# Optimization experiments

Measured on AMD Instinct MI355X. Metric: run time of the kernel, lower is better.

The kernel has to match this reference:

```python
import jax, jax.numpy as jnp
import numpy as np
import math

B, S, D = 8, 2048, 512
H, DH = 8, 64  # heads, head dim

def setup_inputs() -> dict:
    key = jax.random.key(0)
    ks = jax.random.split(key, 13)
    w = 0.02
    return {
        "x_Q": jax.random.normal(ks[0], (B, S, D), jnp.float32),
        "x_K": jax.random.normal(ks[1], (B, S, D), jnp.float32),
        "x_V": jax.random.normal(ks[2], (B, S, D), jnp.float32),
        "Wq": jax.random.normal(ks[3], (H * DH, D), jnp.float32) * w,
        "bq": jnp.zeros((H * DH,), jnp.float32),
        "Wk": jax.random.normal(ks[4], (H * DH, D), jnp.float32) * w,
        "bk": jnp.zeros((H * DH,), jnp.float32),
        "Wv": jax.random.normal(ks[5], (H * DH, D), jnp.float32) * w,
        "bv": jnp.zeros((H * DH,), jnp.float32),
        "Wo": jax.random.normal(ks[6], (D, H * DH), jnp.float32) * w,
        "bo": jnp.zeros((D,), jnp.float32),
        "src_batch_lens": jax.random.randint(ks[7], (B,), 1, S + 1, jnp.int32),
    }

def reference(x_Q, x_K, x_V, Wq, bq, Wk, bk, Wv, bv, Wo, bo, src_batch_lens):
    b, s, _ = x_Q.shape
    # projections (torch Linear: x @ W.T + b), split into heads
    Q = (x_Q @ Wq.T + bq).reshape(b, s, H, DH)
    K = (x_K @ Wk.T + bk).reshape(b, s, H, DH)
    V = (x_V @ Wv.T + bv).reshape(b, s, H, DH)
    scale = 1.0 / math.sqrt(DH)
    # [b, h, q, k] scores
    scores = jnp.einsum('bqhd,bkhd->bhqk', Q * scale, K)
    # padding mask on key positions >= src_batch_lens[i], filled with -1e9
    key_mask = jnp.arange(s)[None, :] >= src_batch_lens[:, None]  # [b, k]
    scores = jnp.where(key_mask[:, None, None, :], -1.0e9, scores)
    attn = jax.nn.softmax(scores, axis=-1)  # dropout p=0.0 -> identity
    ctx = jnp.einsum('bhqk,bkhd->bqhd', attn, V).reshape(b, s, H * DH)
    return ctx @ Wo.T + bo
```

## Files before the change

kernel.cpp:

```cpp
#include <hip/hip_runtime.h>
#include <math.h>

#define NB 8
#define NS 2048
#define ND 512
#define NHH 8
#define NDH 64

typedef __attribute__((ext_vector_type(4))) float f32x4;
typedef __attribute__((ext_vector_type(8))) short bf16x8;
typedef unsigned short ush;

__device__ inline ush f2bf_rne(float f) {
    unsigned u = __float_as_uint(f);
    unsigned r = u + 0x7FFFu + ((u >> 16) & 1u);
    return (ush)(r >> 16);
}
__device__ inline float bf2f(ush h) { return __uint_as_float(((unsigned)h) << 16); }

__device__ inline unsigned cvt_pk_bf16(float lo, float hi) {
    unsigned r;
    asm("v_cvt_pk_bf16_f32 %0, %1, %2" : "=v"(r) : "v"(lo), "v"(hi));
    return r;
}

#if defined(__has_builtin)
#if __has_builtin(__builtin_amdgcn_exp2f)
#define EXP2F(x) __builtin_amdgcn_exp2f(x)
#else
#define EXP2F(x) exp2f(x)
#endif
#else
#define EXP2F(x) exp2f(x)
#endif

#define GLL16(gp, lp) __builtin_amdgcn_global_load_lds( \
    (const __attribute__((address_space(1))) unsigned int*)(gp), \
    (__attribute__((address_space(3))) unsigned int*)(lp), 16, 0, 0)

__global__ __launch_bounds__(256) void conv_w_kernel(
    const float* __restrict__ Wq, const float* __restrict__ Wk,
    const float* __restrict__ Wv, const float* __restrict__ Wo,
    ush* __restrict__ wbf, ush* __restrict__ wo_hi, ush* __restrict__ wo_lo)
{
    const int y = blockIdx.y;
    const int i = (blockIdx.x * 256 + threadIdx.x) * 4;
    if (y < 3) {
        const float* src = (y == 0) ? Wq : (y == 1) ? Wk : Wv;
        const float4 v = *(const float4*)&src[i];
        ushort4 o;
        o.x = f2bf_rne(v.x); o.y = f2bf_rne(v.y);
        o.z = f2bf_rne(v.z); o.w = f2bf_rne(v.w);
        *(ushort4*)&wbf[y * 262144 + i] = o;
    } else {
        const float4 v = *(const float4*)&Wo[i];
        ushort4 hi, lo;
        hi.x = f2bf_rne(v.x); lo.x = f2bf_rne(v.x - bf2f(hi.x));
        hi.y = f2bf_rne(v.y); lo.y = f2bf_rne(v.y - bf2f(hi.y));
        hi.z = f2bf_rne(v.z); lo.z = f2bf_rne(v.z - bf2f(hi.z));
        hi.w = f2bf_rne(v.w); lo.w = f2bf_rne(v.w - bf2f(hi.w));
        *(ushort4*)&wo_hi[i] = hi;
        *(ushort4*)&wo_lo[i] = lo;
    }
}

__global__ __launch_bounds__(256) void qkv_gemm_kernel(
    const float* __restrict__ xq, const float* __restrict__ xk, const float* __restrict__ xv,
    const ush* __restrict__ wbf,
    const float* __restrict__ bq, const float* __restrict__ bk, const float* __restrict__ bv,
    ush* __restrict__ Qb, ush* __restrict__ Kb, ush* __restrict__ VT)
{
    __shared__ ush As[4096];
    __shared__ ush Bs[4096];

    const int z = blockIdx.z;
    const float* X    = (z == 0) ? xq : (z == 1) ? xk : xv;
    const ush*   W    = wbf + z * 262144;
    const float* bias = (z == 0) ? bq : (z == 1) ? bk : bv;

    const int t = threadIdx.x;
    const int w = t >> 6, l = t & 63;
    const int l15 = l & 15, g = l >> 4;
    const int m0 = blockIdx.x * 128, n0 = blockIdx.y * 128;
    const int wm = (w & 1) << 6, wn = (w >> 1) << 6;

    const int srow = l >> 2;
    const int sg   = (l & 3) ^ ((srow + (srow >> 2)) & 3);
    const int fsw  = (g ^ ((l15 + (l15 >> 2)) & 3)) << 3;
    const int c0   = w * 2;

    f32x4 acc[4][4];
    #pragma unroll
    for (int i = 0; i < 4; ++i)
        #pragma unroll
        for (int j = 0; j < 4; ++j) acc[i][j] = (f32x4)(0.0f);

    for (int kt = 0; kt < 512; kt += 32) {
        const size_t ar0 = (size_t)(m0 + c0 * 16 + srow) * 512 + kt + sg * 8;
        const size_t ar1 = (size_t)(m0 + (c0 + 1) * 16 + srow) * 512 + kt + sg * 8;
        const float4 a0 = *(const float4*)&X[ar0];
        const float4 a1 = *(const float4*)&X[ar0 + 4];
        const float4 a2 = *(const float4*)&X[ar1];
        const float4 a3 = *(const float4*)&X[ar1 + 4];

        __syncthreads();

        GLL16(&W[(size_t)(n0 + c0 * 16 + srow) * 512 + kt + sg * 8], &Bs[c0 * 512 + l * 8]);
        GLL16(&W[(size_t)(n0 + (c0 + 1) * 16 + srow) * 512 + kt + sg * 8], &Bs[(c0 + 1) * 512 + l * 8]);

        uint4 u0, u1;
        u0.x = (unsigned)f2bf_rne(a0.x) | ((unsigned)f2bf_rne(a0.y) << 16);
        u0.y = (unsigned)f2bf_rne(a0.z) | ((unsigned)f2bf_rne(a0.w) << 16);
        u0.z = (unsigned)f2bf_rne(a1.x) | ((unsigned)f2bf_rne(a1.y) << 16);
        u0.w = (unsigned)f2bf_rne(a1.z) | ((unsigned)f2bf_rne(a1.w) << 16);
        u1.x = (unsigned)f2bf_rne(a2.x) | ((unsigned)f2bf_rne(a2.y) << 16);
        u1.y = (unsigned)f2bf_rne(a2.z) | ((unsigned)f2bf_rne(a2.w) << 16);
        u1.z = (unsigned)f2bf_rne(a3.x) | ((unsigned)f2bf_rne(a3.y) << 16);
        u1.w = (unsigned)f2bf_rne(a3.z) | ((unsigned)f2bf_rne(a3.w) << 16);
        *(uint4*)&As[c0 * 512 + l * 8] = u0;
        *(uint4*)&As[(c0 + 1) * 512 + l * 8] = u1;

        __syncthreads();

        bf16x8 af[4], bfr[4];
        #pragma unroll
        for (int mi = 0; mi < 4; ++mi)
            af[mi] = *(const bf16x8*)&As[(((w & 1) << 2) + mi) * 512 + l15 * 32 + fsw];
        #pragma unroll
        for (int ni = 0; ni < 4; ++ni)
            bfr[ni] = *(const bf16x8*)&Bs[(((w >> 1) << 2) + ni) * 512 + l15 * 32 + fsw];
        #pragma unroll
        for (int mi = 0; mi < 4; ++mi)
            #pragma unroll
            for (int ni = 0; ni < 4; ++ni)
                acc[mi][ni] = __builtin_amdgcn_mfma_f32_16x16x32_bf16(af[mi], bfr[ni], acc[mi][ni], 0, 0, 0);
    }

    const float qscale = (z == 0) ? 0.18033688011112042f : 1.0f;
    float bnv[4];
    #pragma unroll
    for (int ni = 0; ni < 4; ++ni) bnv[ni] = bias[n0 + wn + ni * 16 + l15];

    if (z < 2) {
        ush* O = (z == 0) ? Qb : Kb;
        #pragma unroll
        for (int mi = 0; mi < 4; ++mi) {
            #pragma unroll
            for (int ni = 0; ni < 4; ++ni) {
                const int n = n0 + wn + ni * 16 + l15;
                const int hh = n >> 6, dh = n & 63;
                #pragma unroll
                for (int r = 0; r < 4; ++r) {
                    const int m = m0 + wm + mi * 16 + (g << 2) + r;
                    const int bi = m >> 11, s = m & (NS - 1);
                    O[((size_t)(bi * 8 + hh) * 2048 + s) * 64 + dh] =
                        f2bf_rne((acc[mi][ni][r] + bnv[ni]) * qscale);
                }
            }
        }
    } else {
        #pragma unroll
        for (int mi = 0; mi < 4; ++mi) {
            #pragma unroll
            for (int ni = 0; ni < 4; ++ni) {
                const int n = n0 + wn + ni * 16 + l15;
                const int hh = n >> 6, dh = n & 63;
                const int mb = m0 + wm + mi * 16 + (g << 2);
                const int bi = mb >> 11, s = mb & (NS - 1);
                ushort4 pk;
                pk.x = f2bf_rne(acc[mi][ni][0] + bnv[ni]);
                pk.y = f2bf_rne(acc[mi][ni][1] + bnv[ni]);
                pk.z = f2bf_rne(acc[mi][ni][2] + bnv[ni]);
                pk.w = f2bf_rne(acc[mi][ni][3] + bnv[ni]);
                *(ushort4*)&VT[((size_t)(bi * 8 + hh) * 64 + dh) * 2048 + s] = pk;
            }
        }
    }
}

__global__ __launch_bounds__(256) void attn_kernel(
    ush* __restrict__ Qb, const ush* __restrict__ Kb,
    const ush* __restrict__ VT, const int* __restrict__ lens,
    ush* __restrict__ ctx_lo)
{
    __shared__ ush Ps[64 * 72];
    __shared__ ush Vt[2 * 4624];

    const int tid = threadIdx.x;
    const int w = tid >> 6, l = tid & 63;
    const int l15 = l & 15, g = l >> 4;

    const int id = blockIdx.x;
    const int h = id & 7, qt = (id >> 3) & 31, b = id >> 8;
    const int L = lens[b];
    const int q0 = qt << 6;
    const size_t bh = ((size_t)b * 8 + h) * 2048;

    const ush* qptr = Qb + (bh + q0 + w * 16 + l15) * 64 + g * 8;
    const bf16x8 qf0 = *(const bf16x8*)(qptr);
    const bf16x8 qf1 = *(const bf16x8*)(qptr + 32);

    const ush* kbase = Kb + (bh + l15) * 64 + g * 8;

    const int dv = tid >> 2, seg = (tid & 3) << 4;
    const ush* vbase = VT + bh * 64 + (size_t)dv * 2048 + seg;
    const int vt_off = dv * 72 + ((dv >> 4) << 3) + seg;

    ush* psw = &Ps[(w * 16 + l15) * 72 + (g << 2)];
    const ush* pp = &Ps[(w * 16 + l15) * 72 + g * 8];

    bf16x8 ones;
    #pragma unroll
    for (int j = 0; j < 8; ++j) ones[j] = (short)0x3F80;

    f32x4 o[4];
    f32x4 ol = (f32x4)(0.0f);
    #pragma unroll
    for (int i = 0; i < 4; ++i) o[i] = (f32x4)(0.0f);

    f32x4 sp[4];
    const int T = (L + 63) >> 6;

    {
        const uint4 v0 = *(const uint4*)(vbase);
        const uint4 v1 = *(const uint4*)(vbase + 8);
        #pragma unroll
        for (int st = 0; st < 4; ++st) sp[st] = (f32x4)(0.0f);
        __builtin_amdgcn_s_setprio(1);
        #pragma unroll
        for (int st = 0; st < 4; ++st) {
            const bf16x8 kf0 = *(const bf16x8*)(kbase + st * 1024);
            const bf16x8 kf1 = *(const bf16x8*)(kbase + st * 1024 + 32);
            sp[st] = __builtin_amdgcn_mfma_f32_16x16x32_bf16(kf0, qf0, sp[st], 0, 0, 0);
            sp[st] = __builtin_amdgcn_mfma_f32_16x16x32_bf16(kf1, qf1, sp[st], 0, 0, 0);
        }
        __builtin_amdgcn_s_setprio(0);
        ush* dst = &Vt[vt_off];
        *(uint4*)dst = v0;
        *(uint4*)(dst + 8) = v1;
        __syncthreads();
    }

    auto finish = [&](const ush* vb, bool masked, int kb0) {
        uint2 pk[4];
        #pragma unroll
        for (int st = 0; st < 4; ++st) {
            float p[4];
            #pragma unroll
            for (int r = 0; r < 4; ++r) {
                float e = EXP2F(sp[st][r]);
                if (masked) {
                    const int key = kb0 + st * 16 + (g << 2) + r;
                    e = (key < L) ? e : 0.0f;
                }
                p[r] = e;
            }
            pk[st].x = cvt_pk_bf16(p[0], p[1]);
            pk[st].y = cvt_pk_bf16(p[2], p[3]);
        }
        #pragma unroll
        for (int st = 0; st < 4; ++st)
            *(uint2*)(psw + st * 16) = pk[st];
        const bf16x8 pf0 = *(const bf16x8*)(pp);
        const bf16x8 pf1 = *(const bf16x8*)(pp + 32);
        __builtin_amdgcn_s_setprio(1);
        ol = __builtin_amdgcn_mfma_f32_16x16x32_bf16(pf0, ones, ol, 0, 0, 0);
        ol = __builtin_amdgcn_mfma_f32_16x16x32_bf16(pf1, ones, ol, 0, 0, 0);
        #pragma unroll
        for (int st2 = 0; st2 < 4; ++st2) {
            const ush* vp = vb + (st2 * 16 + l15) * 72 + (st2 << 3) + g * 8;
            const bf16x8 vf0 = *(const bf16x8*)(vp);
            const bf16x8 vf1 = *(const bf16x8*)(vp + 32);
            o[st2] = __builtin_amdgcn_mfma_f32_16x16x32_bf16(pf0, vf0, o[st2], 0, 0, 0);
            o[st2] = __builtin_amdgcn_mfma_f32_16x16x32_bf16(pf1, vf1, o[st2], 0, 0, 0);
        }
        __builtin_amdgcn_s_setprio(0);
    };

    for (int t = 1; t < T; ++t) {
        const int k0 = t << 6;
        const uint4 nv0 = *(const uint4*)(vbase + k0);
        const uint4 nv1 = *(const uint4*)(vbase + k0 + 8);
        bf16x8 kf[8];
        const ush* kp = kbase + (size_t)k0 * 64;
        #pragma unroll
        for (int st = 0; st < 4; ++st) {
            kf[2 * st]     = *(const bf16x8*)(kp + st * 1024);
            kf[2 * st + 1] = *(const bf16x8*)(kp + st * 1024 + 32);
        }

        finish(&Vt[((t & 1) ^ 1) * 4624], false, 0);

        #pragma unroll
        for (int st = 0; st < 4; ++st) sp[st] = (f32x4)(0.0f);
        __builtin_amdgcn_s_setprio(1);
        #pragma unroll
        for (int st = 0; st < 4; ++st) {
            sp[st] = __builtin_amdgcn_mfma_f32_16x16x32_bf16(kf[2 * st], qf0, sp[st], 0, 0, 0);
            sp[st] = __builtin_amdgcn_mfma_f32_16x16x32_bf16(kf[2 * st + 1], qf1, sp[st], 0, 0, 0);
        }
        __builtin_amdgcn_s_setprio(0);

        ush* dst = &Vt[(t & 1) * 4624 + vt_off];
        *(uint4*)dst = nv0;
        *(uint4*)(dst + 8) = nv1;
        __syncthreads();
    }

    finish(&Vt[((T - 1) & 1) * 4624], true, (T - 1) << 6);

    #pragma unroll
    for (int r = 0; r < 4; ++r) {
        const float inv = 1.0f / ol[r];
        const size_t row = bh + q0 + w * 16 + (g << 2) + r;
        #pragma unroll
        for (int st2 = 0; st2 < 4; ++st2) {
            const float val = o[st2][r] * inv;
            const ush hi = f2bf_rne(val);
            const ush lo = f2bf_rne(val - bf2f(hi));
            Qb[row * 64 + st2 * 16 + l15] = hi;
            ctx_lo[row * 64 + st2 * 16 + l15] = lo;
        }
    }
}

__global__ __launch_bounds__(256) void out_gemm_kernel(
    const ush* __restrict__ ctx_hi, const ush* __restrict__ ctx_lo,
    const ush* __restrict__ wo_hi, const ush* __restrict__ wo_lo,
    const float* __restrict__ bo, float* __restrict__ out)
{
    __shared__ ush Ah[4096], Al[4096], Bh[4096], Bl[4096];

    const int t = threadIdx.x;
    const int w = t >> 6, l = t & 63;
    const int l15 = l & 15, g = l >> 4;
    const int m0 = blockIdx.x * 128, n0 = blockIdx.y * 128;
    const int wm = (w & 1) << 6, wn = (w >> 1) << 6;

    const int srow = l >> 2;
    const int sg   = (l & 3) ^ ((srow + (srow >> 2)) & 3);
    const int fsw  = (g ^ ((l15 + (l15 >> 2)) & 3)) << 3;
    const int c0   = w * 2;

    f32x4 acc[4][4];
    #pragma unroll
    for (int i = 0; i < 4; ++i)
        #pragma unroll
        for (int j = 0; j < 4; ++j) acc[i][j] = (f32x4)(0.0f);

    for (int kt = 0; kt < 512; kt += 32) {
        __syncthreads();
        #pragma unroll
        for (int cc = 0; cc < 2; ++cc) {
            const int c = c0 + cc;
            const int m = m0 + c * 16 + srow;
            const int k = kt + sg * 8;
            const size_t ga = ((size_t)((m >> 11) * 8 + (k >> 6)) * 2048 + (m & (NS - 1))) * 64 + (k & 63);
            GLL16(&ctx_hi[ga], &Ah[c * 512 + l * 8]);
            GLL16(&ctx_lo[ga], &Al[c * 512 + l * 8]);
            const size_t gb = (size_t)(n0 + c * 16 + srow) * 512 + kt + sg * 8;
            GLL16(&wo_hi[gb], &Bh[c * 512 + l * 8]);
            GLL16(&wo_lo[gb], &Bl[c * 512 + l * 8]);
        }
        __syncthreads();

        bf16x8 ah[4], al[4], bh4[4], bl4[4];
        #pragma unroll
        for (int mi = 0; mi < 4; ++mi) {
            const int off = (((w & 1) << 2) + mi) * 512 + l15 * 32 + fsw;
            ah[mi] = *(const bf16x8*)&Ah[off];
            al[mi] = *(const bf16x8*)&Al[off];
        }
        #pragma unroll
        for (int ni = 0; ni < 4; ++ni) {
            const int off = (((w >> 1) << 2) + ni) * 512 + l15 * 32 + fsw;
            bh4[ni] = *(const bf16x8*)&Bh[off];
            bl4[ni] = *(const bf16x8*)&Bl[off];
        }
        #pragma unroll
        for (int mi = 0; mi < 4; ++mi)
            #pragma unroll
            for (int ni = 0; ni < 4; ++ni) {
                acc[mi][ni] = __builtin_amdgcn_mfma_f32_16x16x32_bf16(ah[mi], bh4[ni], acc[mi][ni], 0, 0, 0);
                acc[mi][ni] = __builtin_amdgcn_mfma_f32_16x16x32_bf16(al[mi], bh4[ni], acc[mi][ni], 0, 0, 0);
                acc[mi][ni] = __builtin_amdgcn_mfma_f32_16x16x32_bf16(ah[mi], bl4[ni], acc[mi][ni], 0, 0, 0);
            }
    }

    float bov[4];
    #pragma unroll
    for (int ni = 0; ni < 4; ++ni) bov[ni] = bo[n0 + wn + ni * 16 + l15];

    #pragma unroll
    for (int mi = 0; mi < 4; ++mi)
        #pragma unroll
        for (int ni = 0; ni < 4; ++ni) {
            const int n = n0 + wn + ni * 16 + l15;
            #pragma unroll
            for (int r = 0; r < 4; ++r) {
                const int m = m0 + wm + mi * 16 + (g << 2) + r;
                out[(size_t)m * 512 + n] = acc[mi][ni][r] + bov[ni];
            }
        }
}

extern "C" void kernel_launch(void* const* d_in, const int* in_sizes, int n_in,
                              void* d_out, int out_size, void* d_ws, size_t ws_size,
                              hipStream_t stream)
{
    const float* xq   = (const float*)d_in[0];
    const float* xk   = (const float*)d_in[1];
    const float* xv   = (const float*)d_in[2];
    const float* Wq   = (const float*)d_in[3];
    const float* bq   = (const float*)d_in[4];
    const float* Wk   = (const float*)d_in[5];
    const float* bk   = (const float*)d_in[6];
    const float* Wv   = (const float*)d_in[7];
    const float* bv   = (const float*)d_in[8];
    const float* Wo   = (const float*)d_in[9];
    const float* bo   = (const float*)d_in[10];
    const int*   lens = (const int*)d_in[11];
    float* out = (float*)d_out;

    const size_t elems = (size_t)NB * NHH * NS * NDH;
    ush* Qb     = (ush*)d_ws;
    ush* Kb     = Qb + elems;
    ush* VT     = Kb + elems;
    ush* ctx_lo = VT + elems;
    ush* wbf    = ctx_lo + elems;
    ush* wo_hi  = wbf + 3 * 262144;
    ush* wo_lo  = wo_hi + 262144;

    const dim3 blk(256);
    conv_w_kernel<<<dim3(256, 4), blk, 0, stream>>>(Wq, Wk, Wv, Wo, wbf, wo_hi, wo_lo);
    qkv_gemm_kernel<<<dim3(128, 4, 3), blk, 0, stream>>>(
        xq, xk, xv, wbf, bq, bk, bv, Qb, Kb, VT);
    attn_kernel<<<dim3(NB * NHH * (NS / 64)), blk, 0, stream>>>(Qb, Kb, VT, lens, ctx_lo);
    out_gemm_kernel<<<dim3(128, 4), blk, 0, stream>>>(Qb, ctx_lo, wo_hi, wo_lo, bo, out);
}
```

Measured before the change: 354.8 us.

## Double-buffer GEMM LDS tiles and process 128 queries per attention block

Both projection GEMMs now use double-buffered shared memory, so the next K-tile's global loads (and, in the QKV GEMM, the bf16 conversion) overlap the MFMAs on the current tile, with one barrier per iteration. The attention kernel now has each block handle two 64-row query tiles that share each staged K/V tile, halving K/V reloads and the block count. The cost is doubled LDS per block and more accumulator registers in attention, which may lower occupancy. Fewer attention blocks also makes load imbalance across variable sequence lengths worse.

```diff
diff --git a/kernel.cpp b/kernel.cpp
--- a/kernel.cpp
+++ b/kernel.cpp
@@ -70,8 +70,8 @@
     const float* __restrict__ bq, const float* __restrict__ bk, const float* __restrict__ bv,
     ush* __restrict__ Qb, ush* __restrict__ Kb, ush* __restrict__ VT)
 {
-    __shared__ ush As[4096];
-    __shared__ ush Bs[4096];
+    __shared__ ush As[2][4096];
+    __shared__ ush Bs[2][4096];
 
     const int z = blockIdx.z;
     const float* X    = (z == 0) ? xq : (z == 1) ? xk : xv;
@@ -95,19 +95,15 @@
         #pragma unroll
         for (int j = 0; j < 4; ++j) acc[i][j] = (f32x4)(0.0f);
 
-    for (int kt = 0; kt < 512; kt += 32) {
-        const size_t ar0 = (size_t)(m0 + c0 * 16 + srow) * 512 + kt + sg * 8;
-        const size_t ar1 = (size_t)(m0 + (c0 + 1) * 16 + srow) * 512 + kt + sg * 8;
+    {
+        const size_t ar0 = (size_t)(m0 + c0 * 16 + srow) * 512 + sg * 8;
+        const size_t ar1 = (size_t)(m0 + (c0 + 1) * 16 + srow) * 512 + sg * 8;
         const float4 a0 = *(const float4*)&X[ar0];
         const float4 a1 = *(const float4*)&X[ar0 + 4];
         const float4 a2 = *(const float4*)&X[ar1];
         const float4 a3 = *(const float4*)&X[ar1 + 4];
-
-        __syncthreads();
-
-        GLL16(&W[(size_t)(n0 + c0 * 16 + srow) * 512 + kt + sg * 8], &Bs[c0 * 512 + l * 8]);
-        GLL16(&W[(size_t)(n0 + (c0 + 1) * 16 + srow) * 512 + kt + sg * 8], &Bs[(c0 + 1) * 512 + l * 8]);
-
+        GLL16(&W[(size_t)(n0 + c0 * 16 + srow) * 512 + sg * 8], &Bs[0][c0 * 512 + l * 8]);
+        GLL16(&W[(size_t)(n0 + (c0 + 1) * 16 + srow) * 512 + sg * 8], &Bs[0][(c0 + 1) * 512 + l * 8]);
         uint4 u0, u1;
         u0.x = (unsigned)f2bf_rne(a0.x) | ((unsigned)f2bf_rne(a0.y) << 16);
         u0.y = (unsigned)f2bf_rne(a0.z) | ((unsigned)f2bf_rne(a0.w) << 16);
@@ -117,23 +113,53 @@
         u1.y = (unsigned)f2bf_rne(a2.z) | ((unsigned)f2bf_rne(a2.w) << 16);
         u1.z = (unsigned)f2bf_rne(a3.x) | ((unsigned)f2bf_rne(a3.y) << 16);
         u1.w = (unsigned)f2bf_rne(a3.z) | ((unsigned)f2bf_rne(a3.w) << 16);
-        *(uint4*)&As[c0 * 512 + l * 8] = u0;
-        *(uint4*)&As[(c0 + 1) * 512 + l * 8] = u1;
-
+        *(uint4*)&As[0][c0 * 512 + l * 8] = u0;
+        *(uint4*)&As[0][(c0 + 1) * 512 + l * 8] = u1;
         __syncthreads();
+    }
+
+    for (int ki = 0; ki < 16; ++ki) {
+        const int buf = ki & 1;
+        const int ktn = (ki + 1) * 32;
+        float4 a0, a1, a2, a3;
+        if (ki < 15) {
+            const size_t ar0 = (size_t)(m0 + c0 * 16 + srow) * 512 + ktn + sg * 8;
+            const size_t ar1 = (size_t)(m0 + (c0 + 1) * 16 + srow) * 512 + ktn + sg * 8;
+            a0 = *(const float4*)&X[ar0];
+            a1 = *(const float4*)&X[ar0 + 4];
+            a2 = *(const float4*)&X[ar1];
+            a3 = *(const float4*)&X[ar1 + 4];
+            GLL16(&W[(size_t)(n0 + c0 * 16 + srow) * 512 + ktn + sg * 8], &Bs[buf ^ 1][c0 * 512 + l * 8]);
+            GLL16(&W[(size_t)(n0 + (c0 + 1) * 16 + srow) * 512 + ktn + sg * 8], &Bs[buf ^ 1][(c0 + 1) * 512 + l * 8]);
+        }
 
         bf16x8 af[4], bfr[4];
         #pragma unroll
         for (int mi = 0; mi < 4; ++mi)
-            af[mi] = *(const bf16x8*)&As[(((w & 1) << 2) + mi) * 512 + l15 * 32 + fsw];
+            af[mi] = *(const bf16x8*)&As[buf][(((w & 1) << 2) + mi) * 512 + l15 * 32 + fsw];
         #pragma unroll
         for (int ni = 0; ni < 4; ++ni)
-            bfr[ni] = *(const bf16x8*)&Bs[(((w >> 1) << 2) + ni) * 512 + l15 * 32 + fsw];
+            bfr[ni] = *(const bf16x8*)&Bs[buf][(((w >> 1) << 2) + ni) * 512 + l15 * 32 + fsw];
         #pragma unroll
         for (int mi = 0; mi < 4; ++mi)
             #pragma unroll
             for (int ni = 0; ni < 4; ++ni)
                 acc[mi][ni] = __builtin_amdgcn_mfma_f32_16x16x32_bf16(af[mi], bfr[ni], acc[mi][ni], 0, 0, 0);
+
+        if (ki < 15) {
+            uint4 u0, u1;
+            u0.x = (unsigned)f2bf_rne(a0.x) | ((unsigned)f2bf_rne(a0.y) << 16);
+            u0.y = (unsigned)f2bf_rne(a0.z) | ((unsigned)f2bf_rne(a0.w) << 16);
+            u0.z = (unsigned)f2bf_rne(a1.x) | ((unsigned)f2bf_rne(a1.y) << 16);
+            u0.w = (unsigned)f2bf_rne(a1.z) | ((unsigned)f2bf_rne(a1.w) << 16);
+            u1.x = (unsigned)f2bf_rne(a2.x) | ((unsigned)f2bf_rne(a2.y) << 16);
+            u1.y = (unsigned)f2bf_rne(a2.z) | ((unsigned)f2bf_rne(a2.w) << 16);
+            u1.z = (unsigned)f2bf_rne(a3.x) | ((unsigned)f2bf_rne(a3.y) << 16);
+            u1.w = (unsigned)f2bf_rne(a3.z) | ((unsigned)f2bf_rne(a3.w) << 16);
+            *(uint4*)&As[buf ^ 1][c0 * 512 + l * 8] = u0;
+            *(uint4*)&As[buf ^ 1][(c0 + 1) * 512 + l * 8] = u1;
+        }
+        __syncthreads();
     }
 
     const float qscale = (z == 0) ? 0.18033688011112042f : 1.0f;
@@ -183,7 +209,7 @@
     const ush* __restrict__ VT, const int* __restrict__ lens,
     ush* __restrict__ ctx_lo)
 {
-    __shared__ ush Ps[64 * 72];
+    __shared__ ush Ps[128 * 72];
     __shared__ ush Vt[2 * 4624];
 
     const int tid = threadIdx.x;
@@ -191,14 +217,16 @@
     const int l15 = l & 15, g = l >> 4;
 
     const int id = blockIdx.x;
-    const int h = id & 7, qt = (id >> 3) & 31, b = id >> 8;
+    const int h = id & 7, qt = (id >> 3) & 15, b = id >> 7;
     const int L = lens[b];
-    const int q0 = qt << 6;
+    const int q0 = qt << 7;
     const size_t bh = ((size_t)b * 8 + h) * 2048;
 
     const ush* qptr = Qb + (bh + q0 + w * 16 + l15) * 64 + g * 8;
-    const bf16x8 qf0 = *(const bf16x8*)(qptr);
-    const bf16x8 qf1 = *(const bf16x8*)(qptr + 32);
+    const bf16x8 qfa0 = *(const bf16x8*)(qptr);
+    const bf16x8 qfa1 = *(const bf16x8*)(qptr + 32);
+    const bf16x8 qfb0 = *(const bf16x8*)(qptr + 64 * 64);
+    const bf16x8 qfb1 = *(const bf16x8*)(qptr + 64 * 64 + 32);
 
     const ush* kbase = Kb + (bh + l15) * 64 + g * 8;
 
@@ -206,33 +234,37 @@
     const ush* vbase = VT + bh * 64 + (size_t)dv * 2048 + seg;
     const int vt_off = dv * 72 + ((dv >> 4) << 3) + seg;
 
-    ush* psw = &Ps[(w * 16 + l15) * 72 + (g << 2)];
-    const ush* pp = &Ps[(w * 16 + l15) * 72 + g * 8];
+    ush* psw_a = &Ps[(w * 16 + l15) * 72 + (g << 2)];
+    const ush* pp_a = &Ps[(w * 16 + l15) * 72 + g * 8];
+    ush* psw_b = psw_a + 64 * 72;
+    const ush* pp_b = pp_a + 64 * 72;
 
     bf16x8 ones;
     #pragma unroll
     for (int j = 0; j < 8; ++j) ones[j] = (short)0x3F80;
 
-    f32x4 o[4];
-    f32x4 ol = (f32x4)(0.0f);
-    #pragma unroll
-    for (int i = 0; i < 4; ++i) o[i] = (f32x4)(0.0f);
-
-    f32x4 sp[4];
+    f32x4 oa[4], ob[4];
+    f32x4 ola = (f32x4)(0.0f), olb = (f32x4)(0.0f);
+    #pragma unroll
+    for (int i = 0; i < 4; ++i) { oa[i] = (f32x4)(0.0f); ob[i] = (f32x4)(0.0f); }
+
+    f32x4 spa[4], spb[4];
     const int T = (L + 63) >> 6;
 
     {
         const uint4 v0 = *(const uint4*)(vbase);
         const uint4 v1 = *(const uint4*)(vbase + 8);
         #pragma unroll
-        for (int st = 0; st < 4; ++st) sp[st] = (f32x4)(0.0f);
+        for (int st = 0; st < 4; ++st) { spa[st] = (f32x4)(0.0f); spb[st] = (f32x4)(0.0f); }
         __builtin_amdgcn_s_setprio(1);
         #pragma unroll
         for (int st = 0; st < 4; ++st) {
             const bf16x8 kf0 = *(const bf16x8*)(kbase + st * 1024);
             const bf16x8 kf1 = *(const bf16x8*)(kbase + st * 1024 + 32);
-            sp[st] = __builtin_amdgcn_mfma_f32_16x16x32_bf16(kf0, qf0, sp[st], 0, 0, 0);
-            sp[st] = __builtin_amdgcn_mfma_f32_16x16x32_bf16(kf1, qf1, sp[st], 0, 0, 0);
+            spa[st] = __builtin_amdgcn_mfma_f32_16x16x32_bf16(kf0, qfa0, spa[st], 0, 0, 0);
+            spa[st] = __builtin_amdgcn_mfma_f32_16x16x32_bf16(kf1, qfa1, spa[st], 0, 0, 0);
+            spb[st] = __builtin_amdgcn_mfma_f32_16x16x32_bf16(kf0, qfb0, spb[st], 0, 0, 0);
+            spb[st] = __builtin_amdgcn_mfma_f32_16x16x32_bf16(kf1, qfb1, spb[st], 0, 0, 0);
         }
         __builtin_amdgcn_s_setprio(0);
         ush* dst = &Vt[vt_off];
@@ -242,45 +274,55 @@
     }
 
     auto finish = [&](const ush* vb, bool masked, int kb0) {
-        uint2 pk[4];
+        uint2 pka[4], pkb[4];
         #pragma unroll
         for (int st = 0; st < 4; ++st) {
-            float p[4];
+            float pa[4], pb[4];
             #pragma unroll
             for (int r = 0; r < 4; ++r) {
-                float e = EXP2F(sp[st][r]);
+                float ea = EXP2F(spa[st][r]);
+                float eb = EXP2F(spb[st][r]);
                 if (masked) {
                     const int key = kb0 + st * 16 + (g << 2) + r;
-                    e = (key < L) ? e : 0.0f;
+                    ea = (key < L) ? ea : 0.0f;
+                    eb = (key < L) ? eb : 0.0f;
                 }
-                p[r] = e;
+                pa[r] = ea; pb[r] = eb;
             }
-            pk[st].x = cvt_pk_bf16(p[0], p[1]);
-            pk[st].y = cvt_pk_bf16(p[2], p[3]);
-        }
-        #pragma unroll
-        for (int st = 0; st < 4; ++st)
-            *(uint2*)(psw + st * 16) = pk[st];
-        const bf16x8 pf0 = *(const bf16x8*)(pp);
-        const bf16x8 pf1 = *(const bf16x8*)(pp + 32);
+            pka[st].x = cvt_pk_bf16(pa[0], pa[1]);
+            pka[st].y = cvt_pk_bf16(pa[2], pa[3]);
+            pkb[st].x = cvt_pk_bf16(pb[0], pb[1]);
+            pkb[st].y = cvt_pk_bf16(pb[2], pb[3]);
+        }
+        #pragma unroll
+        for (int st = 0; st < 4; ++st) {
+            *(uint2*)(psw_a + st * 16) = pka[st];
+            *(uint2*)(psw_b + st * 16) = pkb[st];
+        }
+        const bf16x8 pfa0 = *(const bf16x8*)(pp_a);
+        const bf16x8 pfa1 = *(const bf16x8*)(pp_a + 32);
+        const bf16x8 pfb0 = *(const bf16x8*)(pp_b);
+        const bf16x8 pfb1 = *(const bf16x8*)(pp_b + 32);
         __builtin_amdgcn_s_setprio(1);
-        ol = __builtin_amdgcn_mfma_f32_16x16x32_bf16(pf0, ones, ol, 0, 0, 0);
-        ol = __builtin_amdgcn_mfma_f32_16x16x32_bf16(pf1, ones, ol, 0, 0, 0);
+        ola = __builtin_amdgcn_mfma_f32_16x16x32_bf16(pfa0, ones, ola, 0, 0, 0);
+        ola = __builtin_amdgcn_mfma_f32_16x16x32_bf16(pfa1, ones, ola, 0, 0, 0);
+        olb = __builtin_amdgcn_mfma_f32_16x16x32_bf16(pfb0, ones, olb, 0, 0, 0);
+        olb = __builtin_amdgcn_mfma_f32_16x16x32_bf16(pfb1, ones, olb, 0, 0, 0);
         #pragma unroll
         for (int st2 = 0; st2 < 4; ++st2) {
             const ush* vp = vb + (st2 * 16 + l15) * 72 + (st2 << 3) + g * 8;
             const bf16x8 vf0 = *(const bf16x8*)(vp);
             const bf16x8 vf1 = *(const bf16x8*)(vp + 32);
-            o[st2] = __builtin_amdgcn_mfma_f32_16x16x32_bf16(pf0, vf0, o[st2], 0, 0, 0);
-            o[st2] = __builtin_amdgcn_mfma_f32_16x16x32_bf16(pf1, vf1, o[st2], 0, 0, 0);
+            oa[st2] = __builtin_amdgcn_mfma_f32_16x16x32_bf16(pfa0, vf0, oa[st2], 0, 0, 0);
+            oa[st2] = __builtin_amdgcn_mfma_f32_16x16x32_bf16(pfa1, vf1, oa[st2], 0, 0, 0);
+            ob[st2] = __builtin_amdgcn_mfma_f32_16x16x32_bf16(pfb0, vf0, ob[st2], 0, 0, 0);
+            ob[st2] = __builtin_amdgcn_mfma_f32_16x16x32_bf16(pfb1, vf1, ob[st2], 0, 0, 0);
         }
         __builtin_amdgcn_s_setprio(0);
     };
 
     for (int t = 1; t < T; ++t) {
         const int k0 = t << 6;
-        const uint4 nv0 = *(const uint4*)(vbase + k0);
-        const uint4 nv1 = *(const uint4*)(vbase + k0 + 8);
         bf16x8 kf[8];
         const ush* kp = kbase + (size_t)k0 * 64;
         #pragma unroll
@@ -288,16 +330,20 @@
             kf[2 * st]     = *(const bf16x8*)(kp + st * 1024);
             kf[2 * st + 1] = *(const bf16x8*)(kp + st * 1024 + 32);
         }
+        const uint4 nv0 = *(const uint4*)(vbase + k0);
+        const uint4 nv1 = *(const uint4*)(vbase + k0 + 8);
 
         finish(&Vt[((t & 1) ^ 1) * 4624], false, 0);
 
         #pragma unroll
-        for (int st = 0; st < 4; ++st) sp[st] = (f32x4)(0.0f);
+        for (int st = 0; st < 4; ++st) { spa[st] = (f32x4)(0.0f); spb[st] = (f32x4)(0.0f); }
         __builtin_amdgcn_s_setprio(1);
         #pragma unroll
         for (int st = 0; st < 4; ++st) {
-            sp[st] = __builtin_amdgcn_mfma_f32_16x16x32_bf16(kf[2 * st], qf0, sp[st], 0, 0, 0);
-            sp[st] = __builtin_amdgcn_mfma_f32_16x16x32_bf16(kf[2 * st + 1], qf1, sp[st], 0, 0, 0);
+            spa[st] = __builtin_amdgcn_mfma_f32_16x16x32_bf16(kf[2 * st], qfa0, spa[st], 0, 0, 0);
+            spa[st] = __builtin_amdgcn_mfma_f32_16x16x32_bf16(kf[2 * st + 1], qfa1, spa[st], 0, 0, 0);
+            spb[st] = __builtin_amdgcn_mfma_f32_16x16x32_bf16(kf[2 * st], qfb0, spb[st], 0, 0, 0);
+            spb[st] = __builtin_amdgcn_mfma_f32_16x16x32_bf16(kf[2 * st + 1], qfb1, spb[st], 0, 0, 0);
         }
         __builtin_amdgcn_s_setprio(0);
 
@@ -311,15 +357,20 @@
 
     #pragma unroll
     for (int r = 0; r < 4; ++r) {
-        const float inv = 1.0f / ol[r];
-        const size_t row = bh + q0 + w * 16 + (g << 2) + r;
+        const float inva = 1.0f / ola[r];
+        const float invb = 1.0f / olb[r];
+        const size_t rowa = bh + q0 + w * 16 + (g << 2) + r;
+        const size_t rowb = rowa + 64;
         #pragma unroll
         for (int st2 = 0; st2 < 4; ++st2) {
-            const float val = o[st2][r] * inv;
-            const ush hi = f2bf_rne(val);
-            const ush lo = f2bf_rne(val - bf2f(hi));
-            Qb[row * 64 + st2 * 16 + l15] = hi;
-            ctx_lo[row * 64 + st2 * 16 + l15] = lo;
+            const float va = oa[st2][r] * inva;
+            const ush ha = f2bf_rne(va);
+            Qb[rowa * 64 + st2 * 16 + l15] = ha;
+            ctx_lo[rowa * 64 + st2 * 16 + l15] = f2bf_rne(va - bf2f(ha));
+            const float vbv = ob[st2][r] * invb;
+            const ush hb = f2bf_rne(vbv);
+            Qb[rowb * 64 + st2 * 16 + l15] = hb;
+            ctx_lo[rowb * 64 + st2 * 16 + l15] = f2bf_rne(vbv - bf2f(hb));
         }
     }
 }
@@ -329,7 +380,7 @@
     const ush* __restrict__ wo_hi, const ush* __restrict__ wo_lo,
     const float* __restrict__ bo, float* __restrict__ out)
 {
-    __shared__ ush Ah[4096], Al[4096], Bh[4096], Bl[4096];
+    __shared__ ush Ah[2][4096], Al[2][4096], Bh[2][4096], Bl[2][4096];
 
     const int t = threadIdx.x;
     const int w = t >> 6, l = t & 63;
@@ -348,34 +399,40 @@
         #pragma unroll
         for (int j = 0; j < 4; ++j) acc[i][j] = (f32x4)(0.0f);
 
-    for (int kt = 0; kt < 512; kt += 32) {
-        __syncthreads();
+    auto stage = [&](int bf, int kt) {
         #pragma unroll
         for (int cc = 0; cc < 2; ++cc) {
             const int c = c0 + cc;
             const int m = m0 + c * 16 + srow;
             const int k = kt + sg * 8;
             const size_t ga = ((size_t)((m >> 11) * 8 + (k >> 6)) * 2048 + (m & (NS - 1))) * 64 + (k & 63);
-            GLL16(&ctx_hi[ga], &Ah[c * 512 + l * 8]);
-            GLL16(&ctx_lo[ga], &Al[c * 512 + l * 8]);
+            GLL16(&ctx_hi[ga], &Ah[bf][c * 512 + l * 8]);
+            GLL16(&ctx_lo[ga], &Al[bf][c * 512 + l * 8]);
             const size_t gb = (size_t)(n0 + c * 16 + srow) * 512 + kt + sg * 8;
-            GLL16(&wo_hi[gb], &Bh[c * 512 + l * 8]);
-            GLL16(&wo_lo[gb], &Bl[c * 512 + l * 8]);
-        }
-        __syncthreads();
+            GLL16(&wo_hi[gb], &Bh[bf][c * 512 + l * 8]);
+            GLL16(&wo_lo[gb], &Bl[bf][c * 512 + l * 8]);
+        }
+    };
+
+    stage(0, 0);
+    __syncthreads();
+
+    for (int ki = 0; ki < 16; ++ki) {
+        const int buf = ki & 1;
+        if (ki < 15) stage(buf ^ 1, (ki + 1) * 32);
 
         bf16x8 ah[4], al[4], bh4[4], bl4[4];
         #pragma unroll
         for (int mi = 0; mi < 4; ++mi) {
             const int off = (((w & 1) << 2) + mi) * 512 + l15 * 32 + fsw;
-            ah[mi] = *(const bf16x8*)&Ah[off];
-            al[mi] = *(const bf16x8*)&Al[off];
+            ah[mi] = *(const bf16x8*)&Ah[buf][off];
+            al[mi] = *(const bf16x8*)&Al[buf][off];
         }
         #pragma unroll
         for (int ni = 0; ni < 4; ++ni) {
             const int off = (((w >> 1) << 2) + ni) * 512 + l15 * 32 + fsw;
-            bh4[ni] = *(const bf16x8*)&Bh[off];
-            bl4[ni] = *(const bf16x8*)&Bl[off];
+            bh4[ni] = *(const bf16x8*)&Bh[buf][off];
+            bl4[ni] = *(const bf16x8*)&Bl[buf][off];
         }
         #pragma unroll
         for (int mi = 0; mi < 4; ++mi)
@@ -385,6 +442,7 @@
                 acc[mi][ni] = __builtin_amdgcn_mfma_f32_16x16x32_bf16(al[mi], bh4[ni], acc[mi][ni], 0, 0, 0);
                 acc[mi][ni] = __builtin_amdgcn_mfma_f32_16x16x32_bf16(ah[mi], bl4[ni], acc[mi][ni], 0, 0, 0);
             }
+        __syncthreads();
     }
 
     float bov[4];
@@ -435,6 +493,6 @@
     conv_w_kernel<<<dim3(256, 4), blk, 0, stream>>>(Wq, Wk, Wv, Wo, wbf, wo_hi, wo_lo);
     qkv_gemm_kernel<<<dim3(128, 4, 3), blk, 0, stream>>>(
         xq, xk, xv, wbf, bq, bk, bv, Qb, Kb, VT);
-    attn_kernel<<<dim3(NB * NHH * (NS / 64)), blk, 0, stream>>>(Qb, Kb, VT, lens, ctx_lo);
+    attn_kernel<<<dim3(NB * NHH * (NS / 128)), blk, 0, stream>>>(Qb, Kb, VT, lens, ctx_lo);
     out_gemm_kernel<<<dim3(128, 4), blk, 0, stream>>>(Qb, ctx_lo, wo_hi, wo_lo, bo, out);
 }
```

New measurement: 309.8 us. -12.7%, faster.
